# Kernel optimization log

Hardware: AMD Instinct MI355X
Metric: run time of the kernel (lower is better)

## Reference

```python
import jax, jax.numpy as jnp
import numpy as np

ENC = 512   # ENCODER_DIM / card embedding size / LSTM input size
CTX = 512   # context_embeddings width
H = 512     # LSTM hidden size
N = 100000  # num_cards


def _lstm_step(x, h, c, w_ih, w_hh, b_ih, b_hh):
    # PyTorch LSTM gate order: i, f, g, o
    gates = x @ w_ih.T + b_ih + h @ w_hh.T + b_hh
    i, f, g, o = jnp.split(gates, 4, axis=-1)
    c_new = jax.nn.sigmoid(f) * c + jax.nn.sigmoid(i) * jnp.tanh(g)
    h_new = jax.nn.sigmoid(o) * jnp.tanh(c_new)
    return h_new, c_new


def setup_inputs() -> dict:
    key = jax.random.key(0)
    ks = jax.random.split(key, 16)
    s = 0.05
    f32 = jnp.float32
    return {
        "context_embeddings": jax.random.normal(ks[0], (1, CTX), f32),
        "card_embeddings": jax.random.normal(ks[1], (N, ENC), f32),
        "eos_embedding": jax.random.normal(ks[2], (ENC,), f32) * 0.1,
        "ctx_w": jax.random.normal(ks[3], (ENC, CTX), f32) * s,
        "ctx_b": jnp.zeros((ENC,), f32),
        "out_w": jax.random.normal(ks[4], (ENC, H), f32) * s,
        "out_b": jnp.zeros((ENC,), f32),
        "w_ih_0": jax.random.normal(ks[5], (4 * H, ENC), f32) * s,
        "w_hh_0": jax.random.normal(ks[6], (4 * H, H), f32) * s,
        "b_ih_0": jnp.zeros((4 * H,), f32),
        "b_hh_0": jnp.zeros((4 * H,), f32),
        "w_ih_1": jax.random.normal(ks[7], (4 * H, H), f32) * s,
        "w_hh_1": jax.random.normal(ks[8], (4 * H, H), f32) * s,
        "b_ih_1": jnp.zeros((4 * H,), f32),
        "b_hh_1": jnp.zeros((4 * H,), f32),
        "max_selections": 5,
    }


def reference(context_embeddings, card_embeddings, eos_embedding,
              ctx_w, ctx_b, out_w, out_b,
              w_ih_0, w_hh_0, b_ih_0, b_hh_0,
              w_ih_1, w_hh_1, b_ih_1, b_hh_1,
              max_selections):
    temperature = 1.0
    num_cards = card_embeddings.shape[0]
    hid = w_hh_0.shape[1]
    dt = card_embeddings.dtype

    # initial LSTM step on projected context with zero state (seq_len == 1)
    x0 = context_embeddings @ ctx_w.T + ctx_b                     # [1, ENC]
    z = jnp.zeros((1, hid), dt)
    h0, c0 = _lstm_step(x0, z, z, w_ih_0, w_hh_0, b_ih_0, b_hh_0)
    h1, c1 = _lstm_step(h0, z, z, w_ih_1, w_hh_1, b_ih_1, b_hh_1)

    all_emb = jnp.concatenate([card_embeddings, eos_embedding[None, :]], axis=0)  # [N+1, ENC]
    avail = jnp.ones((num_cards,), bool)
    active = jnp.array(True)
    total_log_prob = jnp.asarray(0.0, dt)
    keys = jax.random.split(jax.random.key(42), max_selections)
    card_ids = jnp.arange(num_cards)

    indices = []
    n_steps = min(int(max_selections), num_cards)
    for step in range(n_steps):
        proj = h1 @ out_w.T + out_b                               # [1, ENC]
        card_sims = proj @ card_embeddings.T                      # [1, N]
        eos_sim = proj @ eos_embedding[:, None]                   # [1, 1]
        logits = jnp.concatenate([card_sims, eos_sim], axis=-1)[0] / temperature  # [N+1]
        ext_mask = jnp.concatenate([avail, jnp.ones((1,), bool)])
        logits = jnp.where(ext_mask, logits, -jnp.inf)

        idx = jax.random.categorical(keys[step], logits)          # multinomial(softmax(logits))
        log_prob = jax.nn.log_softmax(logits)[idx]
        total_log_prob = total_log_prob + jnp.where(active, log_prob, jnp.asarray(0.0, dt))

        is_eos = idx == num_cards
        take = active & (~is_eos)
        indices.append(jnp.where(take, idx, -1).astype(jnp.int32))
        avail = avail & ~((card_ids == idx) & take)

        # straight-through one-hot gather of the selected embedding
        hard = jax.nn.one_hot(idx, num_cards + 1, dtype=dt)
        soft = jax.nn.softmax(logits)
        ste = hard + soft - jax.lax.stop_gradient(soft)
        sel_emb = (ste @ all_emb)[None, :]                        # [1, ENC]

        h0, c0 = _lstm_step(sel_emb, h0, c0, w_ih_0, w_hh_0, b_ih_0, b_hh_0)
        h1, c1 = _lstm_step(h0, h1, c1, w_ih_1, w_hh_1, b_ih_1, b_hh_1)
        active = active & (~is_eos)

    selected_indices = jnp.stack(indices)                         # [max_selections], -1 = not selected
    return selected_indices, total_log_prob
```

## Files before the change

### kernel.cpp

```cpp
#include <hip/hip_runtime.h>
#include <stdint.h>
#include <math.h>

#define ENC 512
#define NSTEPS 5
#define NBLK 512
#define NTHR 256
#define NWAVES ((NBLK * NTHR) / 64)
#define ROWS_PER_ITER (NWAVES * 4)
#define FB_BLOCKS 1024
#define FB_WAVES (FB_BLOCKS * 256 / 64)
#define GSTRIDE 100032

struct SelState {
  int   taken[8];
  int   takenCount;
  int   active;
  int   outIdx[8];
  float tlp;
};

struct KParams {
  const float *ctx, *cards, *eos, *ctx_w, *ctx_b, *out_w, *out_b;
  const float *w_ih_0, *w_hh_0, *b_ih_0, *b_hh_0;
  const float *w_ih_1, *w_hh_1, *b_ih_1, *b_hh_1;
  unsigned* bar;
  float* xbuf;
  float* h0s; float* c0s; float* h1s; float* c1s;
  float* projs;
  SelState* st;
  float* bScore; int* bIdxA; float* bLogit; float* bM; float* bS;
  float* gtab;
  float* out;
  int ncards;
  uint32_t k0[NSTEPS], k1[NSTEPS];
};

__host__ __device__ __forceinline__ void tf2x32(uint32_t k0, uint32_t k1,
                                                uint32_t x0, uint32_t x1,
                                                uint32_t& o0, uint32_t& o1) {
  uint32_t ks0 = k0, ks1 = k1, ks2 = k0 ^ k1 ^ 0x1BD11BDAu;
  uint32_t ks[3] = {ks0, ks1, ks2};
  const uint32_t R0[4] = {13u, 15u, 26u, 6u};
  const uint32_t R1[4] = {17u, 29u, 16u, 24u};
  x0 += ks0; x1 += ks1;
#pragma unroll
  for (int i = 0; i < 5; ++i) {
    const uint32_t* r = (i & 1) ? R1 : R0;
#pragma unroll
    for (int j = 0; j < 4; ++j) {
      x0 += x1;
      x1 = (x1 << r[j]) | (x1 >> (32u - r[j]));
      x1 ^= x0;
    }
    x0 += ks[(i + 1) % 3];
    x1 += ks[(i + 2) % 3] + (uint32_t)(i + 1);
  }
  o0 = x0; o1 = x1;
}

__device__ __forceinline__ float gumbel_from_bits(uint32_t bits) {
  float f = __uint_as_float((bits >> 9) | 0x3F800000u) - 1.0f;
  float u = (f == 0.0f) ? 1.17549435e-38f : f;
  return -logf(-logf(u));
}

__device__ __forceinline__ float xla_tanh(float x) {
  if (fabsf(x) < 0.0004f) return x;
  const float kLim = 7.90531110763549805f;
  float cx = fminf(fmaxf(x, -kLim), kLim);
  float x2 = cx * cx;
  float p = -2.76076847742355e-16f;
  p = fmaf(p, x2, 2.00018790482477e-13f);
  p = fmaf(p, x2, -8.60467152213735e-11f);
  p = fmaf(p, x2, 5.12229709037114e-08f);
  p = fmaf(p, x2, 1.48572235717979e-05f);
  p = fmaf(p, x2, 6.37261928875436e-04f);
  p = fmaf(p, x2, 4.89352455891786e-03f);
  p = cx * p;
  float q = 1.19825839466702e-06f;
  q = fmaf(q, x2, 1.18534705686654e-04f);
  q = fmaf(q, x2, 2.26843463243900e-03f);
  q = fmaf(q, x2, 4.89352518554385e-03f);
  return p / q;
}
__device__ __forceinline__ float xla_sigmoid(float x) {
  return 0.5f * xla_tanh(0.5f * x) + 0.5f;
}

__device__ __forceinline__ float dot8(const float4* a, const float4* b, int lane) {
  float4 x0 = a[lane * 2], x1 = a[lane * 2 + 1];
  float4 y0 = b[lane * 2], y1 = b[lane * 2 + 1];
  return x0.x * y0.x + x0.y * y0.y + x0.z * y0.z + x0.w * y0.w +
         x1.x * y1.x + x1.y * y1.y + x1.z * y1.z + x1.w * y1.w;
}
__device__ __forceinline__ float wred(float v) {
#pragma unroll
  for (int k = 1; k < 64; k <<= 1) v += __shfl_xor(v, k, 64);
  return v;
}

__device__ __forceinline__ void cstoref(float* p, float v) {
  __hip_atomic_store(p, v, __ATOMIC_RELAXED, __HIP_MEMORY_SCOPE_AGENT);
}
__device__ __forceinline__ void cstorei(int* p, int v) {
  __hip_atomic_store(p, v, __ATOMIC_RELAXED, __HIP_MEMORY_SCOPE_AGENT);
}

__device__ __forceinline__ void gsync(unsigned* bar, int bid, unsigned target) {
  asm volatile("s_waitcnt vmcnt(0)" ::: "memory");
  __syncthreads();
  const int tid = threadIdx.x;
  unsigned* slots = bar;
  unsigned* rel   = bar + 8192;
  if (tid == 0)
    __hip_atomic_store(&slots[(unsigned)bid * 16u], target,
                       __ATOMIC_RELAXED, __HIP_MEMORY_SCOPE_AGENT);
  if (bid == 0) {
    unsigned* s0 = &slots[(2u * (unsigned)tid) * 16u];
    unsigned* s1 = &slots[(2u * (unsigned)tid + 1u) * 16u];
    while (__hip_atomic_load(s0, __ATOMIC_RELAXED, __HIP_MEMORY_SCOPE_AGENT) < target)
      __builtin_amdgcn_s_sleep(1);
    while (__hip_atomic_load(s1, __ATOMIC_RELAXED, __HIP_MEMORY_SCOPE_AGENT) < target)
      __builtin_amdgcn_s_sleep(1);
    __syncthreads();
    if (tid < 64)
      __hip_atomic_store(&rel[(unsigned)tid * 16u], target,
                         __ATOMIC_RELAXED, __HIP_MEMORY_SCOPE_AGENT);
  } else {
    if (tid == 0) {
      unsigned* r = &rel[((unsigned)bid & 63u) * 16u];
      while (__hip_atomic_load(r, __ATOMIC_RELAXED, __HIP_MEMORY_SCOPE_AGENT) < target)
        __builtin_amdgcn_s_sleep(1);
    }
    __syncthreads();
  }
}

__device__ __forceinline__ void lstm_phase(const float* wih, const float* whh,
                                           const float* bih, const float* bhh,
                                           const float* x, const float* hin, const float* cin,
                                           float* hout, float* cout, float* sG,
                                           int bid, int tid) {
  if (bid < ENC) {
    int g = tid >> 6, lane = tid & 63;
    size_t row = (size_t)(g * ENC + bid) * ENC;
    float accI = dot8((const float4*)(wih + row), (const float4*)x, lane);
    float accH = 0.0f;
    if (hin) accH = dot8((const float4*)(whh + row), (const float4*)hin, lane);
#pragma unroll
    for (int k = 1; k < 64; k <<= 1) {
      accI += __shfl_xor(accI, k, 64);
      accH += __shfl_xor(accH, k, 64);
    }
    if (lane == 0) sG[g] = ((accI + bih[g * ENC + bid]) + accH) + bhh[g * ENC + bid];
    __syncthreads();
    if (tid == 0) {
      float gi = sG[0], gf = sG[1], gg = sG[2], go = sG[3];
      float cprev = cin ? cin[bid] : 0.0f;
      float cn = xla_sigmoid(gf) * cprev + xla_sigmoid(gi) * xla_tanh(gg);
      float hn = xla_sigmoid(go) * xla_tanh(cn);
      cstoref(&cout[bid], cn);
      cstoref(&hout[bid], hn);
    }
  }
}

__global__ __launch_bounds__(NTHR, 2) void mega(KParams P) {
  const int bid = blockIdx.x, tid = threadIdx.x;
  const int wid = tid >> 6, lane = tid & 63;
  const int gw = bid * 4 + wid;
  const int sub = lane & 15;
  const int grp = lane >> 4;
  unsigned ph = 0;

  __shared__ float sG[4];
  __shared__ float fS[NTHR], fL[NTHR], fM[NTHR], fU[NTHR];
  __shared__ int   fI[NTHR];
  __shared__ float wSs[16], wLs[16], wMs[16], wUs[16];
  __shared__ int   wIs[16];
  __shared__ int   sTaken[8];
  __shared__ int   sActive;
  __shared__ float sTlp;
  __shared__ int   sOut[NSTEPS];
  __shared__ int   selSh;

  if (tid == 0) {
    for (int i = 0; i < 8; ++i) sTaken[i] = -1;
    sActive = 1; sTlp = 0.0f;
    for (int i = 0; i < NSTEPS; ++i) sOut[i] = -1;
  }

  const int np1 = P.ncards + 1;
  const int ITERS = (np1 + ROWS_PER_ITER - 1) / ROWS_PER_ITER;

  {
    int total = NSTEPS * np1;
    for (int j = bid * NTHR + tid; j < total; j += NBLK * NTHR) {
      int s = j / np1;
      int i = j - s * np1;
      uint32_t r0, r1;
      tf2x32(P.k0[s], P.k1[s], 0u, (uint32_t)i, r0, r1);
      cstoref(&P.gtab[s * GSTRIDE + i], gumbel_from_bits(r0 ^ r1));
    }
  }
  if (gw >= NWAVES - ENC) {
    int r = gw - (NWAVES - ENC);
    float acc = wred(dot8((const float4*)(P.ctx_w + (size_t)r * ENC), (const float4*)P.ctx, lane));
    if (lane == 0) cstoref(&P.xbuf[r], acc + P.ctx_b[r]);
  }
  gsync(P.bar, bid, ++ph);

  lstm_phase(P.w_ih_0, P.w_hh_0, P.b_ih_0, P.b_hh_0, P.xbuf, nullptr, nullptr,
             P.h0s, P.c0s, sG, bid, tid);
  gsync(P.bar, bid, ++ph);
  lstm_phase(P.w_ih_1, P.w_hh_1, P.b_ih_1, P.b_hh_1, P.h0s, nullptr, nullptr,
             P.h1s, P.c1s, sG, bid, tid);
  gsync(P.bar, bid, ++ph);

  if (gw < ENC) {
    float acc = wred(dot8((const float4*)(P.out_w + (size_t)gw * ENC), (const float4*)P.h1s, lane));
    if (lane == 0) cstoref(&P.projs[gw], acc + P.out_b[gw]);
  }
  gsync(P.bar, bid, ++ph);

  for (int s = 0; s < NSTEPS; ++s) {
    {
      const float4* pv = (const float4*)(P.projs + s * ENC);
      float4 pr[8];
#pragma unroll
      for (int k = 0; k < 8; ++k) pr[k] = pv[sub + 16 * k];
      int t0 = sTaken[0], t1 = sTaken[1], t2 = sTaken[2], t3 = sTaken[3], t4 = sTaken[4];
      const float* gt = P.gtab + s * GSTRIDE;
      float bSc = -INFINITY, bLg = 0.0f, m = -INFINITY, su = 0.0f;
      int bIx = 0x7FFFFFFF;
      for (int t = 0; t < ITERS; ++t) {
        int r = (t * NWAVES + gw) * 4 + grp;
        bool valid = (r < np1);
        const float* rowp = valid ? ((r < P.ncards) ? (P.cards + (size_t)r * ENC) : P.eos)
                                  : P.cards;
        const float4* rv = (const float4*)rowp;
        float4 rr[8];
#pragma unroll
        for (int k = 0; k < 8; ++k) rr[k] = rv[sub + 16 * k];
        float acc = 0.0f;
#pragma unroll
        for (int k = 0; k < 8; ++k)
          acc += rr[k].x * pr[k].x + rr[k].y * pr[k].y + rr[k].z * pr[k].z + rr[k].w * pr[k].w;
        acc += __shfl_xor(acc, 1, 64);
        acc += __shfl_xor(acc, 2, 64);
        acc += __shfl_xor(acc, 4, 64);
        acc += __shfl_xor(acc, 8, 64);
        if (valid && sub == 0) {
          bool masked = (r < P.ncards) &&
                        (r == t0 || r == t1 || r == t2 || r == t3 || r == t4);
          if (!masked) {
            if (acc > m) { su = su * expf(m - acc) + 1.0f; m = acc; }
            else         { su += expf(acc - m); }
            float score = gt[r] + acc;
            if (score > bSc || (score == bSc && r < bIx)) { bSc = score; bIx = r; bLg = acc; }
          }
        }
      }
      if (sub == 0) {
        int q = wid * 4 + grp;
        wSs[q] = bSc; wIs[q] = bIx; wLs[q] = bLg; wMs[q] = m; wUs[q] = su;
      }
      __syncthreads();
      if (tid == 0) {
        float s2 = wSs[0], l2 = wLs[0], m2 = wMs[0], u2 = wUs[0];
        int i2 = wIs[0];
        for (int k = 1; k < 16; ++k) {
          float cs = wSs[k]; int ci = wIs[k];
          if (cs > s2 || (cs == s2 && ci < i2)) { s2 = cs; i2 = ci; l2 = wLs[k]; }
          float cm = wMs[k], cu = wUs[k];
          if (cm > m2) { u2 = u2 * expf(m2 - cm) + cu; m2 = cm; }
          else if (cm > -INFINITY) { u2 += cu * expf(cm - m2); }
        }
        int o = s * NBLK + bid;
        cstoref(&P.bScore[o], s2); cstorei(&P.bIdxA[o], i2);
        cstoref(&P.bLogit[o], l2); cstoref(&P.bM[o], m2); cstoref(&P.bS[o], u2);
      }
    }
    gsync(P.bar, bid, ++ph);

    {
      const float* pSc = P.bScore + s * NBLK;
      const int*   pIx = P.bIdxA  + s * NBLK;
      const float* pLg = P.bLogit + s * NBLK;
      const float* pMm = P.bM     + s * NBLK;
      const float* pSu = P.bS     + s * NBLK;
      float bS2 = -INFINITY, bL2 = 0.0f, m = -INFINITY, su = 0.0f;
      int bI2 = 0x7FFFFFFF;
      for (int i = tid; i < NBLK; i += NTHR) {
        float cs = pSc[i]; int ci = pIx[i];
        if (cs > bS2 || (cs == bS2 && ci < bI2)) { bS2 = cs; bI2 = ci; bL2 = pLg[i]; }
        float cm = pMm[i], cu = pSu[i];
        if (cm > m) { su = su * expf(m - cm) + cu; m = cm; }
        else if (cm > -INFINITY) { su += cu * expf(cm - m); }
      }
      fS[tid] = bS2; fI[tid] = bI2; fL[tid] = bL2; fM[tid] = m; fU[tid] = su;
      __syncthreads();
      for (int off = 128; off > 0; off >>= 1) {
        if (tid < off) {
          float cs = fS[tid + off]; int ci = fI[tid + off];
          if (cs > fS[tid] || (cs == fS[tid] && ci < fI[tid])) {
            fS[tid] = cs; fI[tid] = ci; fL[tid] = fL[tid + off];
          }
          float cm = fM[tid + off], cu = fU[tid + off];
          if (cm > fM[tid]) { fU[tid] = fU[tid] * expf(fM[tid] - cm) + cu; fM[tid] = cm; }
          else if (cm > -INFINITY) { fU[tid] += cu * expf(cm - fM[tid]); }
        }
        __syncthreads();
      }
      if (tid == 0) {
        int idx = fI[0];
        float lse = fM[0] + logf(fU[0]);
        float lp = fL[0] - lse;
        int active = sActive;
        if (active) sTlp += lp;
        int is_eos = (idx == P.ncards);
        int take = active && !is_eos;
        sOut[s] = take ? idx : -1;
        if (take) {
          for (int q = 0; q < 8; ++q) if (sTaken[q] == -1) { sTaken[q] = idx; break; }
        }
        sActive = active && !is_eos;
        selSh = idx;
        if (s == NSTEPS - 1 && bid == 0) {
          for (int q = 0; q < NSTEPS; ++q) P.out[q] = (float)sOut[q];
          P.out[NSTEPS] = sTlp;
        }
      }
      __syncthreads();
    }
    if (s == NSTEPS - 1) break;

    {
      int idx = selSh;
      const float* xrow = (idx < P.ncards) ? (P.cards + (size_t)idx * ENC) : P.eos;
      lstm_phase(P.w_ih_0, P.w_hh_0, P.b_ih_0, P.b_hh_0, xrow,
                 P.h0s + s * ENC, P.c0s + s * ENC,
                 P.h0s + (s + 1) * ENC, P.c0s + (s + 1) * ENC, sG, bid, tid);
    }
    gsync(P.bar, bid, ++ph);
    lstm_phase(P.w_ih_1, P.w_hh_1, P.b_ih_1, P.b_hh_1, P.h0s + (s + 1) * ENC,
               P.h1s + s * ENC, P.c1s + s * ENC,
               P.h1s + (s + 1) * ENC, P.c1s + (s + 1) * ENC, sG, bid, tid);
    gsync(P.bar, bid, ++ph);

    if (gw < ENC) {
      float acc = wred(dot8((const float4*)(P.out_w + (size_t)gw * ENC),
                            (const float4*)(P.h1s + (s + 1) * ENC), lane));
      if (lane == 0) cstoref(&P.projs[(s + 1) * ENC + gw], acc + P.out_b[gw]);
    }
    gsync(P.bar, bid, ++ph);
  }
}

__global__ void init_kernel(float* __restrict__ Z, SelState* st) {
  int t = threadIdx.x;
  if (t < ENC) Z[t] = 0.0f;
  if (t == 0) {
    for (int i = 0; i < 8; ++i) { st->taken[i] = -1; st->outIdx[i] = -1; }
    st->takenCount = 0; st->active = 1; st->tlp = 0.0f;
  }
}

__global__ void gumbel_fill(float* __restrict__ gtab, int ncards,
                            uint32_t k00, uint32_t k01, uint32_t k10, uint32_t k11,
                            uint32_t k20, uint32_t k21, uint32_t k30, uint32_t k31,
                            uint32_t k40, uint32_t k41) {
  uint32_t K0[NSTEPS] = {k00, k10, k20, k30, k40};
  uint32_t K1[NSTEPS] = {k01, k11, k21, k31, k41};
  int np1 = ncards + 1;
  int total = NSTEPS * np1;
  for (int j = blockIdx.x * blockDim.x + threadIdx.x; j < total; j += gridDim.x * blockDim.x) {
    int s = j / np1;
    int i = j - s * np1;
    uint32_t r0, r1;
    tf2x32(K0[s], K1[s], 0u, (uint32_t)i, r0, r1);
    gtab[s * GSTRIDE + i] = gumbel_from_bits(r0 ^ r1);
  }
}

__global__ void matvec512(const float* __restrict__ W, const float* __restrict__ b,
                          const float* __restrict__ vin, float* __restrict__ vout) {
  int tid = blockIdx.x * blockDim.x + threadIdx.x;
  int wave = tid >> 6, lane = tid & 63;
  if (wave >= ENC) return;
  float acc = wred(dot8((const float4*)(W + (size_t)wave * ENC), (const float4*)vin, lane));
  if (lane == 0) vout[wave] = acc + b[wave];
}

__global__ void lstm_step_kernel(const float* __restrict__ w_ih, const float* __restrict__ w_hh,
                                 const float* __restrict__ b_ih, const float* __restrict__ b_hh,
                                 const float* __restrict__ x, const float* __restrict__ h_in,
                                 const float* __restrict__ c_in,
                                 float* __restrict__ h_out, float* __restrict__ c_out) {
  __shared__ float sG[4];
  lstm_phase(w_ih, w_hh, b_ih, b_hh, x, h_in, c_in, h_out, c_out, sG,
             blockIdx.x, threadIdx.x);
}

__global__ void sims_kernel(const float* __restrict__ cards, const float* __restrict__ eos,
                            const float* __restrict__ proj, int ncards,
                            const float* __restrict__ gt,
                            const int* __restrict__ takenList,
                            float* __restrict__ oScore, int* __restrict__ oIdx,
                            float* __restrict__ oLogit, float* __restrict__ oM,
                            float* __restrict__ oS) {
  int tid = blockIdx.x * blockDim.x + threadIdx.x;
  int wave = tid >> 6, lane = tid & 63;
  int nwav = (gridDim.x * blockDim.x) >> 6;
  const float4* pv = (const float4*)proj;
  float4 p0 = pv[lane * 2], p1 = pv[lane * 2 + 1];
  int t0 = takenList[0], t1 = takenList[1], t2 = takenList[2],
      t3 = takenList[3], t4 = takenList[4];
  float bS = -INFINITY, bL = 0.0f, m = -INFINITY, s = 0.0f;
  int bI = 0x7FFFFFFF;
  for (int i = wave; i <= ncards; i += nwav) {
    const float* rowp = (i < ncards) ? (cards + (size_t)i * ENC) : eos;
    const float4* er = (const float4*)rowp;
    float4 e0 = er[lane * 2], e1 = er[lane * 2 + 1];
    float acc = p0.x * e0.x + p0.y * e0.y + p0.z * e0.z + p0.w * e0.w +
                p1.x * e1.x + p1.y * e1.y + p1.z * e1.z + p1.w * e1.w;
    acc = wred(acc);
    bool masked = (i < ncards) &&
                  (i == t0 || i == t1 || i == t2 || i == t3 || i == t4);
    if (!masked) {
      if (acc > m) { s = s * expf(m - acc) + 1.0f; m = acc; }
      else         { s += expf(acc - m); }
      float score = gt[i] + acc;
      if (score > bS || (score == bS && i < bI)) { bS = score; bI = i; bL = acc; }
    }
  }
  if (lane == 0) { oScore[wave] = bS; oIdx[wave] = bI; oLogit[wave] = bL; oM[wave] = m; oS[wave] = s; }
}

__global__ void finalize_kernel(int nw, int step, int ncards,
                                const float* __restrict__ pScore, const int* __restrict__ pIdx,
                                const float* __restrict__ pLogit, const float* __restrict__ pM,
                                const float* __restrict__ pS,
                                const float* __restrict__ cards, const float* __restrict__ eos,
                                SelState* st, float* __restrict__ xout,
                                float* __restrict__ out, int write_out) {
  __shared__ float sS[256], sL[256], sM[256], sU[256];
  __shared__ int sI[256];
  __shared__ int selIdx;
  int t = threadIdx.x;
  float bS = -INFINITY, bL = 0.0f, m = -INFINITY, s = 0.0f;
  int bI = 0x7FFFFFFF;
  for (int i = t; i < nw; i += 256) {
    float cs = pScore[i]; int ci = pIdx[i];
    if (cs > bS || (cs == bS && ci < bI)) { bS = cs; bI = ci; bL = pLogit[i]; }
    float cm = pM[i], cu = pS[i];
    if (cm > m) { s = s * expf(m - cm) + cu; m = cm; }
    else if (cm > -INFINITY) { s += cu * expf(cm - m); }
  }
  sS[t] = bS; sI[t] = bI; sL[t] = bL; sM[t] = m; sU[t] = s;
  __syncthreads();
  for (int off = 128; off > 0; off >>= 1) {
    if (t < off) {
      float cs = sS[t + off]; int ci = sI[t + off];
      if (cs > sS[t] || (cs == sS[t] && ci < sI[t])) { sS[t] = cs; sI[t] = ci; sL[t] = sL[t + off]; }
      float cm = sM[t + off], cu = sU[t + off];
      if (cm > sM[t]) { sU[t] = sU[t] * expf(sM[t] - cm) + cu; sM[t] = cm; }
      else if (cm > -INFINITY) { sU[t] += cu * expf(cm - sM[t]); }
    }
    __syncthreads();
  }
  if (t == 0) {
    int idx = sI[0];
    float lse = sM[0] + logf(sU[0]);
    float lp = sL[0] - lse;
    int active = st->active;
    if (active) st->tlp += lp;
    int is_eos = (idx == ncards);
    int take = active && !is_eos;
    st->outIdx[step] = take ? idx : -1;
    if (take) st->taken[st->takenCount++] = idx;
    st->active = active && !is_eos;
    selIdx = idx;
    if (write_out) {
      for (int q = 0; q < NSTEPS; ++q) out[q] = (float)st->outIdx[q];
      out[NSTEPS] = st->tlp;
    }
  }
  __syncthreads();
  if (!write_out) {
    int idx = selIdx;
    const float* row = (idx < ncards) ? (cards + (size_t)idx * ENC) : eos;
    for (int e = t; e < ENC; e += 256) xout[e] = row[e];
  }
}

extern "C" void kernel_launch(void* const* d_in, const int* in_sizes, int n_in,
                              void* d_out, int out_size, void* d_ws, size_t ws_size,
                              hipStream_t stream) {
  KParams P;
  P.ctx    = (const float*)d_in[0];
  P.cards  = (const float*)d_in[1];
  P.eos    = (const float*)d_in[2];
  P.ctx_w  = (const float*)d_in[3];
  P.ctx_b  = (const float*)d_in[4];
  P.out_w  = (const float*)d_in[5];
  P.out_b  = (const float*)d_in[6];
  P.w_ih_0 = (const float*)d_in[7];
  P.w_hh_0 = (const float*)d_in[8];
  P.b_ih_0 = (const float*)d_in[9];
  P.b_hh_0 = (const float*)d_in[10];
  P.w_ih_1 = (const float*)d_in[11];
  P.w_hh_1 = (const float*)d_in[12];
  P.b_ih_1 = (const float*)d_in[13];
  P.b_hh_1 = (const float*)d_in[14];
  P.ncards = in_sizes[1] / ENC;

  char* wsb = (char*)d_ws;
  P.bar = (unsigned*)wsb;
  float* f = (float*)(wsb + 40960);
  float* Z = f; f += ENC;
  P.xbuf = f; f += ENC;
  P.h0s = f; f += 6 * ENC;
  P.c0s = f; f += 6 * ENC;
  P.h1s = f; f += 6 * ENC;
  P.c1s = f; f += 6 * ENC;
  P.projs = f; f += NSTEPS * ENC;
  P.st = (SelState*)f;  f = (float*)((char*)f + 256);
  P.bScore = f; f += FB_WAVES;
  P.bIdxA = (int*)f; f += FB_WAVES;
  P.bLogit = f; f += FB_WAVES;
  P.bM = f; f += FB_WAVES;
  P.bS = f; f += FB_WAVES;
  P.gtab = f;
  P.out = (float*)d_out;

  for (int s = 0; s < NSTEPS; ++s)
    tf2x32(0u, 42u, 0u, (uint32_t)s, P.k0[s], P.k1[s]);

  hipMemsetAsync(P.bar, 0, 40960, stream);

  void* args[] = { &P };
  hipError_t ce = hipLaunchCooperativeKernel((void*)mega, dim3(NBLK), dim3(NTHR), args, 0, stream);
  if (ce == hipSuccess) return;
  (void)hipGetLastError();

  float* h0A = P.h0s;            float* h0B = P.h0s + ENC;
  float* c0A = P.c0s;            float* c0B = P.c0s + ENC;
  float* h1A = P.h1s;            float* h1B = P.h1s + ENC;
  float* c1A = P.c1s;            float* c1B = P.c1s + ENC;
  float* proj = P.projs;
  float* xbuf = P.xbuf;

  init_kernel<<<1, 512, 0, stream>>>(Z, P.st);
  gumbel_fill<<<512, 256, 0, stream>>>(P.gtab, P.ncards,
                                       P.k0[0], P.k1[0], P.k0[1], P.k1[1], P.k0[2], P.k1[2],
                                       P.k0[3], P.k1[3], P.k0[4], P.k1[4]);
  matvec512<<<128, 256, 0, stream>>>(P.ctx_w, P.ctx_b, P.ctx, xbuf);
  lstm_step_kernel<<<512, 256, 0, stream>>>(P.w_ih_0, P.w_hh_0, P.b_ih_0, P.b_hh_0,
                                            xbuf, Z, Z, h0A, c0A);
  lstm_step_kernel<<<512, 256, 0, stream>>>(P.w_ih_1, P.w_hh_1, P.b_ih_1, P.b_hh_1,
                                            h0A, Z, Z, h1A, c1A);
  float *h0c = h0A, *c0c = c0A, *h1c = h1A, *c1c = c1A;
  float *h0n = h0B, *c0n = c0B, *h1n = h1B, *c1n = c1B;
  for (int s = 0; s < NSTEPS; ++s) {
    matvec512<<<128, 256, 0, stream>>>(P.out_w, P.out_b, h1c, proj);
    sims_kernel<<<FB_BLOCKS, 256, 0, stream>>>(P.cards, P.eos, proj, P.ncards,
                                               P.gtab + s * GSTRIDE, (const int*)P.st,
                                               P.bScore, P.bIdxA, P.bLogit, P.bM, P.bS);
    finalize_kernel<<<1, 256, 0, stream>>>(FB_WAVES, s, P.ncards,
                                           P.bScore, P.bIdxA, P.bLogit, P.bM, P.bS,
                                           P.cards, P.eos, P.st, xbuf,
                                           P.out, (s == NSTEPS - 1) ? 1 : 0);
    if (s == NSTEPS - 1) break;
    lstm_step_kernel<<<512, 256, 0, stream>>>(P.w_ih_0, P.w_hh_0, P.b_ih_0, P.b_hh_0,
                                              xbuf, h0c, c0c, h0n, c0n);
    lstm_step_kernel<<<512, 256, 0, stream>>>(P.w_ih_1, P.w_hh_1, P.b_ih_1, P.b_hh_1,
                                              h0n, h1c, c1c, h1n, c1n);
    float* tp;
    tp = h0c; h0c = h0n; h0n = tp;
    tp = c0c; c0c = c0n; c0n = tp;
    tp = h1c; h1c = h1n; h1n = tp;
    tp = c1c; c1c = c1n; c1n = tp;
  }
}
```

Measured before the change: 284.5 us.

## Split grid barrier into arrive/wait, prefetch weights across barriers, unroll scan by two

The grid barrier is split into arrive and waitall. Every block now polls all arrival slots directly instead of waiting on a release flag written by block 0. Between arrive and wait, each block prefetches the LSTM and output-projection weights, biases and previous state it will need next, so those loads overlap the barrier latency. The card-scoring scan now handles two rows per 16-lane group per iteration, which gives more loads in flight. The cost is more atomic polling traffic, since all 512 blocks read the slots, and higher register pressure.

```diff
diff --git a/kernel.cpp b/kernel.cpp
--- a/kernel.cpp
+++ b/kernel.cpp
@@ -7,7 +7,7 @@
 #define NBLK 512
 #define NTHR 256
 #define NWAVES ((NBLK * NTHR) / 64)
-#define ROWS_PER_ITER (NWAVES * 4)
+#define ROWS_PER_ITER (NWAVES * 8)
 #define FB_BLOCKS 1024
 #define FB_WAVES (FB_BLOCKS * 256 / 64)
 #define GSTRIDE 100032
@@ -107,34 +107,26 @@
   __hip_atomic_store(p, v, __ATOMIC_RELAXED, __HIP_MEMORY_SCOPE_AGENT);
 }
 
-__device__ __forceinline__ void gsync(unsigned* bar, int bid, unsigned target) {
+__device__ __forceinline__ void arrive(unsigned* bar, int bid, unsigned target) {
   asm volatile("s_waitcnt vmcnt(0)" ::: "memory");
   __syncthreads();
+  if (threadIdx.x == 0)
+    __hip_atomic_store(&bar[(unsigned)bid * 16u], target,
+                       __ATOMIC_RELAXED, __HIP_MEMORY_SCOPE_AGENT);
+}
+__device__ __forceinline__ void waitall(unsigned* bar, unsigned target) {
   const int tid = threadIdx.x;
-  unsigned* slots = bar;
-  unsigned* rel   = bar + 8192;
-  if (tid == 0)
-    __hip_atomic_store(&slots[(unsigned)bid * 16u], target,
-                       __ATOMIC_RELAXED, __HIP_MEMORY_SCOPE_AGENT);
-  if (bid == 0) {
-    unsigned* s0 = &slots[(2u * (unsigned)tid) * 16u];
-    unsigned* s1 = &slots[(2u * (unsigned)tid + 1u) * 16u];
-    while (__hip_atomic_load(s0, __ATOMIC_RELAXED, __HIP_MEMORY_SCOPE_AGENT) < target)
-      __builtin_amdgcn_s_sleep(1);
-    while (__hip_atomic_load(s1, __ATOMIC_RELAXED, __HIP_MEMORY_SCOPE_AGENT) < target)
-      __builtin_amdgcn_s_sleep(1);
-    __syncthreads();
-    if (tid < 64)
-      __hip_atomic_store(&rel[(unsigned)tid * 16u], target,
-                         __ATOMIC_RELAXED, __HIP_MEMORY_SCOPE_AGENT);
-  } else {
-    if (tid == 0) {
-      unsigned* r = &rel[((unsigned)bid & 63u) * 16u];
-      while (__hip_atomic_load(r, __ATOMIC_RELAXED, __HIP_MEMORY_SCOPE_AGENT) < target)
-        __builtin_amdgcn_s_sleep(1);
-    }
-    __syncthreads();
-  }
+  unsigned* s0 = &bar[(2u * (unsigned)tid) * 16u];
+  unsigned* s1 = &bar[(2u * (unsigned)tid + 1u) * 16u];
+  while (__hip_atomic_load(s0, __ATOMIC_RELAXED, __HIP_MEMORY_SCOPE_AGENT) < target)
+    __builtin_amdgcn_s_sleep(1);
+  while (__hip_atomic_load(s1, __ATOMIC_RELAXED, __HIP_MEMORY_SCOPE_AGENT) < target)
+    __builtin_amdgcn_s_sleep(1);
+  __syncthreads();
+}
+__device__ __forceinline__ void gsync(unsigned* bar, int bid, unsigned target) {
+  arrive(bar, bid, target);
+  waitall(bar, target);
 }
 
 __device__ __forceinline__ void lstm_phase(const float* wih, const float* whh,
@@ -172,6 +164,7 @@
   const int gw = bid * 4 + wid;
   const int sub = lane & 15;
   const int grp = lane >> 4;
+  const int g = wid;
   unsigned ph = 0;
 
   __shared__ float sG[4];
@@ -235,30 +228,49 @@
       float bSc = -INFINITY, bLg = 0.0f, m = -INFINITY, su = 0.0f;
       int bIx = 0x7FFFFFFF;
       for (int t = 0; t < ITERS; ++t) {
-        int r = (t * NWAVES + gw) * 4 + grp;
-        bool valid = (r < np1);
-        const float* rowp = valid ? ((r < P.ncards) ? (P.cards + (size_t)r * ENC) : P.eos)
-                                  : P.cards;
-        const float4* rv = (const float4*)rowp;
-        float4 rr[8];
-#pragma unroll
-        for (int k = 0; k < 8; ++k) rr[k] = rv[sub + 16 * k];
-        float acc = 0.0f;
-#pragma unroll
-        for (int k = 0; k < 8; ++k)
-          acc += rr[k].x * pr[k].x + rr[k].y * pr[k].y + rr[k].z * pr[k].z + rr[k].w * pr[k].w;
-        acc += __shfl_xor(acc, 1, 64);
-        acc += __shfl_xor(acc, 2, 64);
-        acc += __shfl_xor(acc, 4, 64);
-        acc += __shfl_xor(acc, 8, 64);
-        if (valid && sub == 0) {
-          bool masked = (r < P.ncards) &&
-                        (r == t0 || r == t1 || r == t2 || r == t3 || r == t4);
-          if (!masked) {
-            if (acc > m) { su = su * expf(m - acc) + 1.0f; m = acc; }
-            else         { su += expf(acc - m); }
-            float score = gt[r] + acc;
-            if (score > bSc || (score == bSc && r < bIx)) { bSc = score; bIx = r; bLg = acc; }
+        int base = (t * NWAVES + gw) * 8;
+        int rA = base + grp;
+        int rB = base + 4 + grp;
+        bool vA = (rA < np1), vB = (rB < np1);
+        const float* rpA = vA ? ((rA < P.ncards) ? (P.cards + (size_t)rA * ENC) : P.eos) : P.cards;
+        const float* rpB = vB ? ((rB < P.ncards) ? (P.cards + (size_t)rB * ENC) : P.eos) : P.cards;
+        const float4* ra = (const float4*)rpA;
+        const float4* rb = (const float4*)rpB;
+        float4 rrA[8], rrB[8];
+#pragma unroll
+        for (int k = 0; k < 8; ++k) { rrA[k] = ra[sub + 16 * k]; rrB[k] = rb[sub + 16 * k]; }
+        float gA = vA ? gt[rA] : 0.0f;
+        float gB = vB ? gt[rB] : 0.0f;
+        float accA = 0.0f, accB = 0.0f;
+#pragma unroll
+        for (int k = 0; k < 8; ++k) {
+          accA += rrA[k].x * pr[k].x + rrA[k].y * pr[k].y + rrA[k].z * pr[k].z + rrA[k].w * pr[k].w;
+          accB += rrB[k].x * pr[k].x + rrB[k].y * pr[k].y + rrB[k].z * pr[k].z + rrB[k].w * pr[k].w;
+        }
+        accA += __shfl_xor(accA, 1, 64); accB += __shfl_xor(accB, 1, 64);
+        accA += __shfl_xor(accA, 2, 64); accB += __shfl_xor(accB, 2, 64);
+        accA += __shfl_xor(accA, 4, 64); accB += __shfl_xor(accB, 4, 64);
+        accA += __shfl_xor(accA, 8, 64); accB += __shfl_xor(accB, 8, 64);
+        if (sub == 0) {
+          if (vA) {
+            bool masked = (rA < P.ncards) &&
+                          (rA == t0 || rA == t1 || rA == t2 || rA == t3 || rA == t4);
+            if (!masked) {
+              if (accA > m) { su = su * expf(m - accA) + 1.0f; m = accA; }
+              else          { su += expf(accA - m); }
+              float score = gA + accA;
+              if (score > bSc || (score == bSc && rA < bIx)) { bSc = score; bIx = rA; bLg = accA; }
+            }
+          }
+          if (vB) {
+            bool masked = (rB < P.ncards) &&
+                          (rB == t0 || rB == t1 || rB == t2 || rB == t3 || rB == t4);
+            if (!masked) {
+              if (accB > m) { su = su * expf(m - accB) + 1.0f; m = accB; }
+              else          { su += expf(accB - m); }
+              float score = gB + accB;
+              if (score > bSc || (score == bSc && rB < bIx)) { bSc = score; bIx = rB; bLg = accB; }
+            }
           }
         }
       }
@@ -282,7 +294,23 @@
         cstoref(&P.bLogit[o], l2); cstoref(&P.bM[o], m2); cstoref(&P.bS[o], u2);
       }
     }
-    gsync(P.bar, bid, ++ph);
+    arrive(P.bar, bid, ++ph);
+    if (s == NSTEPS - 1 && bid != 0) return;
+
+    float4 dwa, dwb, dva, dvb, dha, dhb;
+    float dbi = 0.0f, dbh = 0.0f, dci = 0.0f;
+    if (s < NSTEPS - 1) {
+      size_t row = (size_t)(g * ENC + bid) * ENC;
+      const float4* wi = (const float4*)(P.w_ih_0 + row);
+      const float4* wh = (const float4*)(P.w_hh_0 + row);
+      dwa = wi[lane * 2]; dwb = wi[lane * 2 + 1];
+      dva = wh[lane * 2]; dvb = wh[lane * 2 + 1];
+      const float4* hv = (const float4*)(P.h0s + s * ENC);
+      dha = hv[lane * 2]; dhb = hv[lane * 2 + 1];
+      dbi = P.b_ih_0[g * ENC + bid]; dbh = P.b_hh_0[g * ENC + bid];
+      dci = P.c0s[s * ENC + bid];
+    }
+    waitall(P.bar, ph);
 
     {
       const float* pSc = P.bScore + s * NBLK;
@@ -339,19 +367,79 @@
     {
       int idx = selSh;
       const float* xrow = (idx < P.ncards) ? (P.cards + (size_t)idx * ENC) : P.eos;
-      lstm_phase(P.w_ih_0, P.w_hh_0, P.b_ih_0, P.b_hh_0, xrow,
-                 P.h0s + s * ENC, P.c0s + s * ENC,
-                 P.h0s + (s + 1) * ENC, P.c0s + (s + 1) * ENC, sG, bid, tid);
-    }
-    gsync(P.bar, bid, ++ph);
-    lstm_phase(P.w_ih_1, P.w_hh_1, P.b_ih_1, P.b_hh_1, P.h0s + (s + 1) * ENC,
-               P.h1s + s * ENC, P.c1s + s * ENC,
-               P.h1s + (s + 1) * ENC, P.c1s + (s + 1) * ENC, sG, bid, tid);
-    gsync(P.bar, bid, ++ph);
-
+      const float4* xv = (const float4*)xrow;
+      float4 xa = xv[lane * 2], xb = xv[lane * 2 + 1];
+      float accI = dwa.x * xa.x + dwa.y * xa.y + dwa.z * xa.z + dwa.w * xa.w +
+                   dwb.x * xb.x + dwb.y * xb.y + dwb.z * xb.z + dwb.w * xb.w;
+      float accH = dva.x * dha.x + dva.y * dha.y + dva.z * dha.z + dva.w * dha.w +
+                   dvb.x * dhb.x + dvb.y * dhb.y + dvb.z * dhb.z + dvb.w * dhb.w;
+#pragma unroll
+      for (int k = 1; k < 64; k <<= 1) {
+        accI += __shfl_xor(accI, k, 64);
+        accH += __shfl_xor(accH, k, 64);
+      }
+      if (lane == 0) sG[g] = ((accI + dbi) + accH) + dbh;
+      __syncthreads();
+      if (tid == 0) {
+        float gi = sG[0], gf = sG[1], gg = sG[2], go = sG[3];
+        float cn = xla_sigmoid(gf) * dci + xla_sigmoid(gi) * xla_tanh(gg);
+        float hn = xla_sigmoid(go) * xla_tanh(cn);
+        cstoref(&P.c0s[(s + 1) * ENC + bid], cn);
+        cstoref(&P.h0s[(s + 1) * ENC + bid], hn);
+      }
+    }
+    arrive(P.bar, bid, ++ph);
+    float4 ewa, ewb, eva, evb, eha, ehb;
+    float ebi, ebh, eci;
+    {
+      size_t row = (size_t)(g * ENC + bid) * ENC;
+      const float4* wi = (const float4*)(P.w_ih_1 + row);
+      const float4* wh = (const float4*)(P.w_hh_1 + row);
+      ewa = wi[lane * 2]; ewb = wi[lane * 2 + 1];
+      eva = wh[lane * 2]; evb = wh[lane * 2 + 1];
+      const float4* hv = (const float4*)(P.h1s + s * ENC);
+      eha = hv[lane * 2]; ehb = hv[lane * 2 + 1];
+      ebi = P.b_ih_1[g * ENC + bid]; ebh = P.b_hh_1[g * ENC + bid];
+      eci = P.c1s[s * ENC + bid];
+    }
+    waitall(P.bar, ph);
+
+    {
+      const float4* xv = (const float4*)(P.h0s + (s + 1) * ENC);
+      float4 xa = xv[lane * 2], xb = xv[lane * 2 + 1];
+      float accI = ewa.x * xa.x + ewa.y * xa.y + ewa.z * xa.z + ewa.w * xa.w +
+                   ewb.x * xb.x + ewb.y * xb.y + ewb.z * xb.z + ewb.w * xb.w;
+      float accH = eva.x * eha.x + eva.y * eha.y + eva.z * eha.z + eva.w * eha.w +
+                   evb.x * ehb.x + evb.y * ehb.y + evb.z * ehb.z + evb.w * ehb.w;
+#pragma unroll
+      for (int k = 1; k < 64; k <<= 1) {
+        accI += __shfl_xor(accI, k, 64);
+        accH += __shfl_xor(accH, k, 64);
+      }
+      if (lane == 0) sG[g] = ((accI + ebi) + accH) + ebh;
+      __syncthreads();
+      if (tid == 0) {
+        float gi = sG[0], gf = sG[1], gg = sG[2], go = sG[3];
+        float cn = xla_sigmoid(gf) * eci + xla_sigmoid(gi) * xla_tanh(gg);
+        float hn = xla_sigmoid(go) * xla_tanh(cn);
+        cstoref(&P.c1s[(s + 1) * ENC + bid], cn);
+        cstoref(&P.h1s[(s + 1) * ENC + bid], hn);
+      }
+    }
+    arrive(P.bar, bid, ++ph);
+    float4 awa, awb;
     if (gw < ENC) {
-      float acc = wred(dot8((const float4*)(P.out_w + (size_t)gw * ENC),
-                            (const float4*)(P.h1s + (s + 1) * ENC), lane));
+      const float4* ow = (const float4*)(P.out_w + (size_t)gw * ENC);
+      awa = ow[lane * 2]; awb = ow[lane * 2 + 1];
+    }
+    waitall(P.bar, ph);
+
+    if (gw < ENC) {
+      const float4* hv = (const float4*)(P.h1s + (s + 1) * ENC);
+      float4 ha = hv[lane * 2], hb = hv[lane * 2 + 1];
+      float acc = awa.x * ha.x + awa.y * ha.y + awa.z * ha.z + awa.w * ha.w +
+                  awb.x * hb.x + awb.y * hb.y + awb.z * hb.z + awb.w * hb.w;
+      acc = wred(acc);
       if (lane == 0) cstoref(&P.projs[(s + 1) * ENC + gw], acc + P.out_b[gw]);
     }
     gsync(P.bar, bid, ++ph);
```

Result: slower. 312.9 us (+10.0%).
